# Optimization experiments

Measured on AMD Instinct MI355X. Metric: run time of the kernel, lower is better.

Reference implementation:

```python
import jax, jax.numpy as jnp
import numpy as np

B, T, V, E, H = 16, 32, 1003, 100, 2048


def setup_inputs() -> dict:
    key = jax.random.key(0)
    ks = jax.random.split(key, 16)
    s = 0.02
    n = lambda k, shape: (jax.random.normal(k, shape, jnp.float32) * s)
    tokens = jax.random.randint(ks[0], (B, T), 0, V, dtype=jnp.int32)
    return {
        "tokens": tokens,
        "emb": n(ks[1], (V, E)),
        "W1": n(ks[2], (E, 4 * H)), "U1": n(ks[3], (H, 4 * H)), "b1": jnp.zeros((4 * H,), jnp.float32),
        "W2": n(ks[4], (H, 4 * H)), "U2": n(ks[5], (H, 4 * H)), "b2": jnp.zeros((4 * H,), jnp.float32),
        "W3": n(ks[6], (H, 4 * H)), "U3": n(ks[7], (H, 4 * H)), "b3": jnp.zeros((4 * H,), jnp.float32),
        "Wd1": n(ks[8], (H, H)), "bd1": jnp.zeros((H,), jnp.float32),
        "Wd2": n(ks[9], (H, V)), "bd2": jnp.zeros((V,), jnp.float32),
    }


def masked_lstm(x, mask, W, U, b):
    """Keras-semantics masked LSTM. x: [B,T,D], mask: [B,T] bool.
    Masked steps carry h,c through unchanged (cuDNN-incompatible path).
    Returns (all_h: [B,T,H], last_h: [B,H])."""
    Hd = U.shape[0]
    Bd = x.shape[0]
    # precompute input projections for all timesteps at once: [T,B,4H]
    xz = jnp.einsum('btd,dh->tbh', x, W) + b
    m_t = jnp.swapaxes(mask, 0, 1)  # [T,B]

    def step(carry, inp):
        h, c = carry
        zx, mt = inp
        z = zx + h @ U  # [B,4H]
        i, f, g, o = jnp.split(z, 4, axis=-1)
        i = jax.nn.sigmoid(i)
        f = jax.nn.sigmoid(f)
        g = jnp.tanh(g)
        o = jax.nn.sigmoid(o)
        c_new = f * c + i * g
        h_new = o * jnp.tanh(c_new)
        m = mt[:, None]
        h_new = jnp.where(m, h_new, h)
        c_new = jnp.where(m, c_new, c)
        return (h_new, c_new), h_new

    init = (jnp.zeros((Bd, Hd), x.dtype), jnp.zeros((Bd, Hd), x.dtype))
    (h_last, _), hs = jax.lax.scan(step, init, (xz, m_t))
    return jnp.swapaxes(hs, 0, 1), h_last


def reference(tokens, emb, W1, U1, b1, W2, U2, b2, W3, U3, b3, Wd1, bd1, Wd2, bd2):
    mask = tokens != 0  # mask_zero=True semantics
    x = emb[tokens]  # [B,T,E]
    x, _ = masked_lstm(x, mask, W1, U1, b1)
    x, _ = masked_lstm(x, mask, W2, U2, b2)
    _, h = masked_lstm(x, mask, W3, U3, b3)  # return_sequences=False -> last (carried) state
    y = h @ Wd1 + bd1  # Dense, linear activation
    logits = y @ Wd2 + bd2
    return jax.nn.softmax(logits, axis=-1)
```

## Files before the change

kernel.cpp:

```cpp
#include <hip/hip_runtime.h>
#include <hip/hip_bf16.h>
#include <cstddef>

#define BB 16
#define TT 32
#define VV 1003
#define EE 100
#define HH 2048
#define G4 8192

typedef __attribute__((ext_vector_type(4))) float f32x4;
typedef unsigned char u8;

#define SA 64.0f
#define SB 128.0f
#define DESCALE 1.220703125e-4f

__device__ __forceinline__ unsigned pk_lo(unsigned old, float a, float b) {
  return (unsigned)__builtin_amdgcn_cvt_pk_fp8_f32(a, b, (int)old, false);
}
__device__ __forceinline__ unsigned pk_hi(unsigned old, float a, float b) {
  return (unsigned)__builtin_amdgcn_cvt_pk_fp8_f32(a, b, (int)old, true);
}
__device__ __forceinline__ u8 cvt1fp8(float a) {
  return (u8)(__builtin_amdgcn_cvt_pk_fp8_f32(a, 0.f, 0, false) & 0xff);
}

__global__ __launch_bounds__(256) void embed_frag(
    const int* __restrict__ tokens, const float* __restrict__ emb,
    u8* __restrict__ xf) {
  int i = blockIdx.x * 256 + threadIdx.x;
  if (i >= TT * BB * 128) return;
  int e = i & 127, b = (i >> 7) & 15, t = i >> 11;
  float v = 0.f;
  if (e < EE) v = emb[(size_t)tokens[b * TT + t] * EE + e] * SA;
  int kt = e >> 5, kk = e & 31;
  int lane = (kk >> 3) * 16 + b, j = kk & 7;
  xf[(size_t)t * 2048 + ((size_t)kt * 64 + lane) * 8 + j] = cvt1fp8(v);
}

__global__ __launch_bounds__(256) void split_fp8(
    const float* __restrict__ src, u8* __restrict__ dst,
    int Kreal, int nkt) {
  __shared__ float ld[32][257];
  int tid = threadIdx.x;
  int kt = blockIdx.x, ct0 = blockIdx.y * 16;
  int r0 = kt * 32;

#pragma unroll
  for (int i = 0; i < 8; i++) {
    int elem = i * 1024 + tid * 4;
    int row = elem >> 8, c = elem & 255;
    int g = c >> 6, rel = c & 63;
    int r = r0 + row;
    float4 v = make_float4(0.f, 0.f, 0.f, 0.f);
    if (r < Kreal)
      v = *(const float4*)&src[(size_t)r * G4 + (size_t)g * HH + ct0 * 4 + rel];
    ld[row][c] = v.x; ld[row][c + 1] = v.y;
    ld[row][c + 2] = v.z; ld[row][c + 3] = v.w;
  }
  __syncthreads();

  int L = tid & 63;
  int cl = L & 15, g = cl >> 2, hq = cl & 3;
  int row0 = (L >> 4) * 8;
#pragma unroll
  for (int pass = 0; pass < 4; pass++) {
    int ctr = (tid >> 6) + pass * 4;
    int col = g * 64 + ctr * 4 + hq;
    unsigned lo = 0, hi = 0;
    lo = pk_lo(lo, ld[row0 + 0][col] * SB, ld[row0 + 1][col] * SB);
    lo = pk_hi(lo, ld[row0 + 2][col] * SB, ld[row0 + 3][col] * SB);
    hi = pk_lo(hi, ld[row0 + 4][col] * SB, ld[row0 + 5][col] * SB);
    hi = pk_hi(hi, ld[row0 + 6][col] * SB, ld[row0 + 7][col] * SB);
    *(uint2*)&dst[((size_t)(ct0 + ctr) * nkt + kt) * 512 + L * 8] =
        make_uint2(lo, hi);
  }
}

__global__ __launch_bounds__(512) void gemm_mfma(
    const u8* __restrict__ af, int t_stride, int nkt,
    const u8* __restrict__ wfrag, const float* __restrict__ bias,
    float* __restrict__ xz) {
  __shared__ __align__(16) u8 Bs[3][2][8][512];
  int tid = threadIdx.x;
  int w = tid >> 6, L = tid & 63;
  int ct0 = blockIdx.x * 8;
  int t_a = blockIdx.y * 4 + (w & 3);
  int nt0 = (w >> 2) * 4;

  f32x4 acc[4];
#pragma unroll
  for (int i = 0; i < 4; i++) acc[i] = (f32x4){0.f, 0.f, 0.f, 0.f};
  const u8* Ah = af + (size_t)t_a * t_stride + L * 8;
  int ns = nkt >> 1;

  int tl = tid >> 5, off = (tid & 31) * 16;
  int s_nt = tl >> 1, s_kk = tl & 1;

  {
    uint4 t0 = *(const uint4*)&wfrag[((size_t)(ct0 + s_nt) * nkt + s_kk) * 512 + off];
    *(uint4*)&Bs[0][s_kk][s_nt][off] = t0;
    if (ns > 1) {
      uint4 t1 = *(const uint4*)&wfrag[((size_t)(ct0 + s_nt) * nkt + 2 + s_kk) * 512 + off];
      *(uint4*)&Bs[1][s_kk][s_nt][off] = t1;
    }
  }
  __syncthreads();

  for (int s = 0; s < ns; s++) {
    uint4 nx;
    bool pf = (s + 2 < ns);
    if (pf)
      nx = *(const uint4*)&wfrag[((size_t)(ct0 + s_nt) * nkt + 2 * (s + 2) + s_kk) * 512 + off];
    int buf = s % 3;
#pragma unroll
    for (int kk = 0; kk < 2; kk++) {
      long aH = *(const long*)(Ah + (size_t)(2 * s + kk) * 512);
#pragma unroll
      for (int i = 0; i < 4; i++) {
        long bH = *(const long*)&Bs[buf][kk][nt0 + i][L * 8];
        acc[i] = __builtin_amdgcn_mfma_f32_16x16x32_fp8_fp8(aH, bH, acc[i], 0, 0, 0);
      }
    }
    if (pf) *(uint4*)&Bs[(s + 2) % 3][s_kk][s_nt][off] = nx;
    __syncthreads();
  }

  int nq = L >> 4, hl = L & 15;
#pragma unroll
  for (int i = 0; i < 4; i++) {
    int ctg = ct0 + nt0 + i;
    int gcol = (hl >> 2) * HH + ctg * 4 + (hl & 3);
    float bv = bias[gcol];
#pragma unroll
    for (int r = 0; r < 4; r++) {
      int b = nq * 4 + r;
      xz[((size_t)t_a * 16 + b) * G4 + ctg * 16 + hl] = acc[i][r] * DESCALE + bv;
    }
  }
}

__global__ __launch_bounds__(512, 4) void lstm_step(
    const u8* __restrict__ Ufrag,
    const float* __restrict__ xzt,
    const u8* __restrict__ hf_in,
    u8* __restrict__ hf_out,
    const float* __restrict__ hT_in,
    float* __restrict__ hT_out,
    float* __restrict__ c,
    const int* __restrict__ tokens, int t) {
  __shared__ float red[8][16][16];
  __shared__ float zs[16][16];
  int tid = threadIdx.x, w = tid >> 6, L = tid & 63;
  int ct = blockIdx.x;

  float xzv = 0.f;
  if (tid < 256) xzv = xzt[(size_t)(tid >> 4) * G4 + ct * 16 + (tid & 15)];
  float c_old = 0.f, h_old = 0.f;
  int tok = 1;
  if (tid < 64) {
    int b = tid >> 2, hq = tid & 3;
    int hu = ct * 4 + hq;
    c_old = c[(size_t)b * HH + hu];
    h_old = hT_in[(size_t)hu * BB + b];
    tok = tokens[b * TT + t];
  }

  f32x4 acc = {0.f, 0.f, 0.f, 0.f};
  const u8* Ub = Ufrag + ((size_t)ct * 64 + w * 8) * 512 + L * 8;
  const u8* Hb = hf_in + (size_t)(w * 8) * 512 + L * 8;

#pragma unroll
  for (int i = 0; i < 8; i++) {
    long bh = *(const long*)(Ub + i * 512);
    long ah = *(const long*)(Hb + i * 512);
    acc = __builtin_amdgcn_mfma_f32_16x16x32_fp8_fp8(ah, bh, acc, 0, 0, 0);
  }
#pragma unroll
  for (int r = 0; r < 4; r++) red[w][(L >> 4) * 4 + r][L & 15] = acc[r];
  __syncthreads();

  if (tid < 256) {
    int b = tid >> 4, cl = tid & 15;
    float s = 0.f;
#pragma unroll
    for (int q = 0; q < 8; q++) s += red[q][b][cl];
    zs[b][cl] = s * DESCALE + xzv;
  }
  __syncthreads();

  if (tid < 64) {
    int b = tid >> 2, hq = tid & 3;
    int hu = ct * 4 + hq;
    float z0 = zs[b][0 + hq];
    float z1 = zs[b][4 + hq];
    float z2 = zs[b][8 + hq];
    float z3 = zs[b][12 + hq];
    float ig = 1.f / (1.f + expf(-z0));
    float fg = 1.f / (1.f + expf(-z1));
    float gt = tanhf(z2);
    float og = 1.f / (1.f + expf(-z3));
    float cn = fg * c_old + ig * gt;
    float hn = og * tanhf(cn);
    if (tok == 0) {
      cn = c_old;
      hn = h_old;
    }
    c[(size_t)b * HH + hu] = cn;
    hT_out[(size_t)hu * BB + b] = hn;
    int kt2 = hu >> 5, kk = hu & 31;
    int lane2 = (kk >> 3) * 16 + b, jj = kk & 7;
    hf_out[((size_t)kt2 * 64 + lane2) * 8 + jj] = cvt1fp8(hn * SA);
  }
}

__global__ __launch_bounds__(256) void head_partial(
    const float* __restrict__ XT, const float* __restrict__ W,
    float* __restrict__ partial, int N) {
  __shared__ float xs[4096];
  int tid = threadIdx.x;
  int k0 = blockIdx.y * 256;
  const float* src = XT + (size_t)k0 * 16;
  for (int i = tid; i < 4096; i += 256) xs[i] = src[i];
  __syncthreads();
  int kg = tid >> 6, lane = tid & 63;
  int col = blockIdx.x * 64 + lane;
  if (col >= N) return;
  float acc[16];
#pragma unroll
  for (int b = 0; b < 16; b++) acc[b] = 0.f;
  const float* Wp = W + (size_t)(k0 + kg * 64) * N + col;
  const float* xp = xs + kg * 64 * 16;
  for (int kk = 0; kk < 64; kk++) {
    float wv = Wp[(size_t)kk * N];
#pragma unroll
    for (int b = 0; b < 16; b++) acc[b] = fmaf(xp[kk * 16 + b], wv, acc[b]);
  }
  int chunk = blockIdx.y * 4 + kg;
#pragma unroll
  for (int b = 0; b < 16; b++)
    partial[((size_t)chunk * 16 + b) * N + col] = acc[b];
}

__global__ __launch_bounds__(256) void head_reduce(
    const float* __restrict__ partial, const float* __restrict__ bias,
    float* __restrict__ out, int N, int sc, int sb) {
  int i = blockIdx.x * 256 + threadIdx.x;
  if (i >= 16 * N) return;
  int b = i / N, col = i - b * N;
  float s = bias[col];
#pragma unroll 8
  for (int ch = 0; ch < 32; ch++) s += partial[((size_t)ch * 16 + b) * N + col];
  out[(size_t)col * sc + (size_t)b * sb] = s;
}

__global__ __launch_bounds__(256) void softmax_rows(
    const float* __restrict__ logits, float* __restrict__ out, int N) {
  __shared__ float buf[1024];
  __shared__ float wred[4];
  __shared__ float rmax, rsum;
  int b = blockIdx.x, tid = threadIdx.x;
  float m = -1e30f;
  for (int v = tid; v < N; v += 256) {
    float x = logits[(size_t)b * N + v];
    buf[v] = x;
    m = fmaxf(m, x);
  }
  for (int o = 32; o > 0; o >>= 1) m = fmaxf(m, __shfl_down(m, o, 64));
  if ((tid & 63) == 0) wred[tid >> 6] = m;
  __syncthreads();
  if (tid == 0) rmax = fmaxf(fmaxf(wred[0], wred[1]), fmaxf(wred[2], wred[3]));
  __syncthreads();
  float s = 0.f;
  for (int v = tid; v < N; v += 256) {
    float e = expf(buf[v] - rmax);
    buf[v] = e;
    s += e;
  }
  for (int o = 32; o > 0; o >>= 1) s += __shfl_down(s, o, 64);
  if ((tid & 63) == 0) wred[tid >> 6] = s;
  __syncthreads();
  if (tid == 0) rsum = wred[0] + wred[1] + wred[2] + wred[3];
  __syncthreads();
  float inv = 1.f / rsum;
  for (int v = tid; v < N; v += 256) out[(size_t)b * N + v] = buf[v] * inv;
}

extern "C" void kernel_launch(void* const* d_in, const int* in_sizes, int n_in,
                              void* d_out, int out_size, void* d_ws, size_t ws_size,
                              hipStream_t stream) {
  const int*   tokens = (const int*)d_in[0];
  const float* emb  = (const float*)d_in[1];
  const float* W1   = (const float*)d_in[2];
  const float* U1   = (const float*)d_in[3];
  const float* b1   = (const float*)d_in[4];
  const float* W2   = (const float*)d_in[5];
  const float* U2   = (const float*)d_in[6];
  const float* b2   = (const float*)d_in[7];
  const float* W3   = (const float*)d_in[8];
  const float* U3   = (const float*)d_in[9];
  const float* b3   = (const float*)d_in[10];
  const float* Wd1  = (const float*)d_in[11];
  const float* bd1  = (const float*)d_in[12];
  const float* Wd2  = (const float*)d_in[13];
  const float* bd2  = (const float*)d_in[14];
  float* out = (float*)d_out;

  char* base = (char*)d_ws;
  size_t off = 0;
  auto carve = [&](size_t bytes) -> char* {
    char* p = base + off;
    off += (bytes + 255) & ~(size_t)255;
    return p;
  };
  float* xz      = (float*)carve((size_t)TT * BB * G4 * 4);
  u8*    allhf0  = (u8*)carve(33ull * 32768);
  u8*    allhf1  = (u8*)carve(33ull * 32768);
  u8*    allhf2  = (u8*)carve(33ull * 32768);
  u8*    xfrag   = (u8*)carve((size_t)TT * 2048);
  u8*    wfrag   = (u8*)carve(512ull * 64 * 512);
  u8*    ufrag   = (u8*)carve(512ull * 64 * 512);
  float* hT0     = (float*)carve(2 * HH * BB * 4);
  float* cbuf    = hT0 + HH * BB;
  float* hT1     = (float*)carve(HH * BB * 4);
  float* yT      = (float*)carve(HH * BB * 4);
  float* logits  = (float*)carve(BB * 1024 * 4);
  float* partial = (float*)carve(32ull * 16 * HH * 4);

  u8* allhf[3] = {allhf0, allhf1, allhf2};
  const float* Us[3] = {U1, U2, U3};
  const float* Ws[3] = {W1, W2, W3};
  const float* bs[3] = {b1, b2, b3};
  float* hping[2] = {hT0, hT1};

  embed_frag<<<dim3(256), 256, 0, stream>>>(tokens, emb, xfrag);

  for (int layer = 0; layer < 3; layer++) {
    const u8* af;
    int t_stride, nktW, KrealW;
    if (layer == 0) {
      af = xfrag; t_stride = 2048; nktW = 4; KrealW = EE;
    } else {
      af = allhf[layer - 1] + 32768;
      t_stride = 32768; nktW = 64; KrealW = HH;
    }
    split_fp8<<<dim3(nktW, 32), 256, 0, stream>>>(Ws[layer], wfrag, KrealW, nktW);
    gemm_mfma<<<dim3(64, 8), 512, 0, stream>>>(
        af, t_stride, nktW, wfrag, bs[layer], xz);
    split_fp8<<<dim3(64, 32), 256, 0, stream>>>(Us[layer], ufrag, HH, 64);

    (void)hipMemsetAsync(allhf[layer], 0, 32768, stream);
    (void)hipMemsetAsync(hT0, 0, 2 * HH * BB * 4, stream);
    for (int t = 0; t < TT; t++) {
      lstm_step<<<dim3(512), 512, 0, stream>>>(
          ufrag, xz + (size_t)t * BB * G4,
          allhf[layer] + (size_t)t * 32768, allhf[layer] + (size_t)(t + 1) * 32768,
          hping[t & 1], hping[(t + 1) & 1], cbuf, tokens, t);
    }
  }

  head_partial<<<dim3(HH / 64, 8), 256, 0, stream>>>(hT0, Wd1, partial, HH);
  head_reduce<<<dim3((16 * HH + 255) / 256), 256, 0, stream>>>(partial, bd1, yT, HH, 16, 1);
  head_partial<<<dim3((VV + 63) / 64, 8), 256, 0, stream>>>(yT, Wd2, partial, VV);
  head_reduce<<<dim3((16 * VV + 255) / 256), 256, 0, stream>>>(partial, bd2, logits, VV, 1, VV);
  softmax_rows<<<dim3(BB), 256, 0, stream>>>(logits, out, VV);
}
```

Baseline: 667.0 us.

## Pair fp8 K-tiles into 16-byte fragments and split head GEMM K finer

Changes the fp8 fragment layout so each lane holds two consecutive 32-wide K tiles in 16 contiguous bytes. The split, gemm and LSTM step kernels then issue one 128-bit load per two MFMAs instead of two 64-bit loads, which cuts the load instruction count in the latency-bound recurrent step. Separately, the dense head splits K into 64 chunks instead of 32 to launch more blocks. That doubles the partial-sum buffer and the reduction work in exchange.

```diff
diff --git a/kernel.cpp b/kernel.cpp
--- a/kernel.cpp
+++ b/kernel.cpp
@@ -24,6 +24,9 @@
 }
 __device__ __forceinline__ u8 cvt1fp8(float a) {
   return (u8)(__builtin_amdgcn_cvt_pk_fp8_f32(a, 0.f, 0, false) & 0xff);
+}
+__device__ __forceinline__ long mklong(unsigned lo, unsigned hi) {
+  return (long)(((unsigned long long)hi << 32) | lo);
 }
 
 __global__ __launch_bounds__(256) void embed_frag(
@@ -36,19 +39,20 @@
   if (e < EE) v = emb[(size_t)tokens[b * TT + t] * EE + e] * SA;
   int kt = e >> 5, kk = e & 31;
   int lane = (kk >> 3) * 16 + b, j = kk & 7;
-  xf[(size_t)t * 2048 + ((size_t)kt * 64 + lane) * 8 + j] = cvt1fp8(v);
+  xf[(size_t)t * 2048 + (size_t)(kt >> 1) * 1024 + lane * 16 + (kt & 1) * 8 + j] =
+      cvt1fp8(v);
 }
 
 __global__ __launch_bounds__(256) void split_fp8(
     const float* __restrict__ src, u8* __restrict__ dst,
-    int Kreal, int nkt) {
-  __shared__ float ld[32][257];
+    int Kreal, int nkt2) {
+  __shared__ float ld[64][257];
   int tid = threadIdx.x;
-  int kt = blockIdx.x, ct0 = blockIdx.y * 16;
-  int r0 = kt * 32;
-
-#pragma unroll
-  for (int i = 0; i < 8; i++) {
+  int pair = blockIdx.x, ct0 = blockIdx.y * 16;
+  int r0 = pair * 64;
+
+#pragma unroll
+  for (int i = 0; i < 16; i++) {
     int elem = i * 1024 + tid * 4;
     int row = elem >> 8, c = elem & 255;
     int g = c >> 6, rel = c & 63;
@@ -68,21 +72,25 @@
   for (int pass = 0; pass < 4; pass++) {
     int ctr = (tid >> 6) + pass * 4;
     int col = g * 64 + ctr * 4 + hq;
-    unsigned lo = 0, hi = 0;
-    lo = pk_lo(lo, ld[row0 + 0][col] * SB, ld[row0 + 1][col] * SB);
-    lo = pk_hi(lo, ld[row0 + 2][col] * SB, ld[row0 + 3][col] * SB);
-    hi = pk_lo(hi, ld[row0 + 4][col] * SB, ld[row0 + 5][col] * SB);
-    hi = pk_hi(hi, ld[row0 + 6][col] * SB, ld[row0 + 7][col] * SB);
-    *(uint2*)&dst[((size_t)(ct0 + ctr) * nkt + kt) * 512 + L * 8] =
-        make_uint2(lo, hi);
+    unsigned lo0 = 0, hi0 = 0, lo1 = 0, hi1 = 0;
+    lo0 = pk_lo(lo0, ld[row0 + 0][col] * SB, ld[row0 + 1][col] * SB);
+    lo0 = pk_hi(lo0, ld[row0 + 2][col] * SB, ld[row0 + 3][col] * SB);
+    hi0 = pk_lo(hi0, ld[row0 + 4][col] * SB, ld[row0 + 5][col] * SB);
+    hi0 = pk_hi(hi0, ld[row0 + 6][col] * SB, ld[row0 + 7][col] * SB);
+    lo1 = pk_lo(lo1, ld[32 + row0 + 0][col] * SB, ld[32 + row0 + 1][col] * SB);
+    lo1 = pk_hi(lo1, ld[32 + row0 + 2][col] * SB, ld[32 + row0 + 3][col] * SB);
+    hi1 = pk_lo(hi1, ld[32 + row0 + 4][col] * SB, ld[32 + row0 + 5][col] * SB);
+    hi1 = pk_hi(hi1, ld[32 + row0 + 6][col] * SB, ld[32 + row0 + 7][col] * SB);
+    *(uint4*)&dst[((size_t)(ct0 + ctr) * nkt2 + pair) * 1024 + L * 16] =
+        make_uint4(lo0, hi0, lo1, hi1);
   }
 }
 
 __global__ __launch_bounds__(512) void gemm_mfma(
-    const u8* __restrict__ af, int t_stride, int nkt,
+    const u8* __restrict__ af, int t_stride, int nkt2,
     const u8* __restrict__ wfrag, const float* __restrict__ bias,
     float* __restrict__ xz) {
-  __shared__ __align__(16) u8 Bs[3][2][8][512];
+  __shared__ __align__(16) u8 Bs[3][8][1024];
   int tid = threadIdx.x;
   int w = tid >> 6, L = tid & 63;
   int ct0 = blockIdx.x * 8;
@@ -92,38 +100,35 @@
   f32x4 acc[4];
 #pragma unroll
   for (int i = 0; i < 4; i++) acc[i] = (f32x4){0.f, 0.f, 0.f, 0.f};
-  const u8* Ah = af + (size_t)t_a * t_stride + L * 8;
-  int ns = nkt >> 1;
-
-  int tl = tid >> 5, off = (tid & 31) * 16;
-  int s_nt = tl >> 1, s_kk = tl & 1;
+  const u8* Ah = af + (size_t)t_a * t_stride + L * 16;
+
+  int s_nt = tid >> 6, boff = (tid & 63) * 16;
 
   {
-    uint4 t0 = *(const uint4*)&wfrag[((size_t)(ct0 + s_nt) * nkt + s_kk) * 512 + off];
-    *(uint4*)&Bs[0][s_kk][s_nt][off] = t0;
-    if (ns > 1) {
-      uint4 t1 = *(const uint4*)&wfrag[((size_t)(ct0 + s_nt) * nkt + 2 + s_kk) * 512 + off];
-      *(uint4*)&Bs[1][s_kk][s_nt][off] = t1;
-    }
-  }
-  __syncthreads();
-
-  for (int s = 0; s < ns; s++) {
+    uint4 t0 = *(const uint4*)&wfrag[((size_t)(ct0 + s_nt) * nkt2 + 0) * 1024 + boff];
+    *(uint4*)&Bs[0][s_nt][boff] = t0;
+    if (nkt2 > 1) {
+      uint4 t1 = *(const uint4*)&wfrag[((size_t)(ct0 + s_nt) * nkt2 + 1) * 1024 + boff];
+      *(uint4*)&Bs[1][s_nt][boff] = t1;
+    }
+  }
+  __syncthreads();
+
+  for (int s = 0; s < nkt2; s++) {
     uint4 nx;
-    bool pf = (s + 2 < ns);
+    bool pf = (s + 2 < nkt2);
     if (pf)
-      nx = *(const uint4*)&wfrag[((size_t)(ct0 + s_nt) * nkt + 2 * (s + 2) + s_kk) * 512 + off];
+      nx = *(const uint4*)&wfrag[((size_t)(ct0 + s_nt) * nkt2 + s + 2) * 1024 + boff];
     int buf = s % 3;
-#pragma unroll
-    for (int kk = 0; kk < 2; kk++) {
-      long aH = *(const long*)(Ah + (size_t)(2 * s + kk) * 512);
-#pragma unroll
-      for (int i = 0; i < 4; i++) {
-        long bH = *(const long*)&Bs[buf][kk][nt0 + i][L * 8];
-        acc[i] = __builtin_amdgcn_mfma_f32_16x16x32_fp8_fp8(aH, bH, acc[i], 0, 0, 0);
-      }
-    }
-    if (pf) *(uint4*)&Bs[(s + 2) % 3][s_kk][s_nt][off] = nx;
+    uint4 a = *(const uint4*)(Ah + (size_t)s * 1024);
+    long a0 = mklong(a.x, a.y), a1 = mklong(a.z, a.w);
+#pragma unroll
+    for (int i = 0; i < 4; i++) {
+      uint4 bb = *(const uint4*)&Bs[buf][nt0 + i][L * 16];
+      acc[i] = __builtin_amdgcn_mfma_f32_16x16x32_fp8_fp8(a0, mklong(bb.x, bb.y), acc[i], 0, 0, 0);
+      acc[i] = __builtin_amdgcn_mfma_f32_16x16x32_fp8_fp8(a1, mklong(bb.z, bb.w), acc[i], 0, 0, 0);
+    }
+    if (pf) *(uint4*)&Bs[(s + 2) % 3][s_nt][boff] = nx;
     __syncthreads();
   }
 
@@ -168,14 +173,15 @@
   }
 
   f32x4 acc = {0.f, 0.f, 0.f, 0.f};
-  const u8* Ub = Ufrag + ((size_t)ct * 64 + w * 8) * 512 + L * 8;
-  const u8* Hb = hf_in + (size_t)(w * 8) * 512 + L * 8;
-
-#pragma unroll
-  for (int i = 0; i < 8; i++) {
-    long bh = *(const long*)(Ub + i * 512);
-    long ah = *(const long*)(Hb + i * 512);
-    acc = __builtin_amdgcn_mfma_f32_16x16x32_fp8_fp8(ah, bh, acc, 0, 0, 0);
+  const u8* Ub = Ufrag + ((size_t)ct * 32 + w * 4) * 1024 + L * 16;
+  const u8* Hb = hf_in + (size_t)(w * 4) * 1024 + L * 16;
+
+#pragma unroll
+  for (int i = 0; i < 4; i++) {
+    uint4 u = *(const uint4*)(Ub + i * 1024);
+    uint4 h = *(const uint4*)(Hb + i * 1024);
+    acc = __builtin_amdgcn_mfma_f32_16x16x32_fp8_fp8(mklong(h.x, h.y), mklong(u.x, u.y), acc, 0, 0, 0);
+    acc = __builtin_amdgcn_mfma_f32_16x16x32_fp8_fp8(mklong(h.z, h.w), mklong(u.z, u.w), acc, 0, 0, 0);
   }
 #pragma unroll
   for (int r = 0; r < 4; r++) red[w][(L >> 4) * 4 + r][L & 15] = acc[r];
@@ -211,18 +217,19 @@
     hT_out[(size_t)hu * BB + b] = hn;
     int kt2 = hu >> 5, kk = hu & 31;
     int lane2 = (kk >> 3) * 16 + b, jj = kk & 7;
-    hf_out[((size_t)kt2 * 64 + lane2) * 8 + jj] = cvt1fp8(hn * SA);
+    hf_out[(size_t)(kt2 >> 1) * 1024 + lane2 * 16 + (kt2 & 1) * 8 + jj] =
+        cvt1fp8(hn * SA);
   }
 }
 
 __global__ __launch_bounds__(256) void head_partial(
     const float* __restrict__ XT, const float* __restrict__ W,
     float* __restrict__ partial, int N) {
-  __shared__ float xs[4096];
+  __shared__ float xs[2048];
   int tid = threadIdx.x;
-  int k0 = blockIdx.y * 256;
+  int k0 = blockIdx.y * 128;
   const float* src = XT + (size_t)k0 * 16;
-  for (int i = tid; i < 4096; i += 256) xs[i] = src[i];
+  for (int i = tid; i < 2048; i += 256) xs[i] = src[i];
   __syncthreads();
   int kg = tid >> 6, lane = tid & 63;
   int col = blockIdx.x * 64 + lane;
@@ -230,9 +237,9 @@
   float acc[16];
 #pragma unroll
   for (int b = 0; b < 16; b++) acc[b] = 0.f;
-  const float* Wp = W + (size_t)(k0 + kg * 64) * N + col;
-  const float* xp = xs + kg * 64 * 16;
-  for (int kk = 0; kk < 64; kk++) {
+  const float* Wp = W + (size_t)(k0 + kg * 32) * N + col;
+  const float* xp = xs + kg * 32 * 16;
+  for (int kk = 0; kk < 32; kk++) {
     float wv = Wp[(size_t)kk * N];
 #pragma unroll
     for (int b = 0; b < 16; b++) acc[b] = fmaf(xp[kk * 16 + b], wv, acc[b]);
@@ -251,7 +258,7 @@
   int b = i / N, col = i - b * N;
   float s = bias[col];
 #pragma unroll 8
-  for (int ch = 0; ch < 32; ch++) s += partial[((size_t)ch * 16 + b) * N + col];
+  for (int ch = 0; ch < 64; ch++) s += partial[((size_t)ch * 16 + b) * N + col];
   out[(size_t)col * sc + (size_t)b * sb] = s;
 }
 
@@ -326,7 +333,7 @@
   float* hT1     = (float*)carve(HH * BB * 4);
   float* yT      = (float*)carve(HH * BB * 4);
   float* logits  = (float*)carve(BB * 1024 * 4);
-  float* partial = (float*)carve(32ull * 16 * HH * 4);
+  float* partial = (float*)carve(64ull * 16 * HH * 4);
 
   u8* allhf[3] = {allhf0, allhf1, allhf2};
   const float* Us[3] = {U1, U2, U3};
@@ -338,17 +345,17 @@
 
   for (int layer = 0; layer < 3; layer++) {
     const u8* af;
-    int t_stride, nktW, KrealW;
+    int t_stride, nkt2W, KrealW;
     if (layer == 0) {
-      af = xfrag; t_stride = 2048; nktW = 4; KrealW = EE;
+      af = xfrag; t_stride = 2048; nkt2W = 2; KrealW = EE;
     } else {
       af = allhf[layer - 1] + 32768;
-      t_stride = 32768; nktW = 64; KrealW = HH;
-    }
-    split_fp8<<<dim3(nktW, 32), 256, 0, stream>>>(Ws[layer], wfrag, KrealW, nktW);
+      t_stride = 32768; nkt2W = 32; KrealW = HH;
+    }
+    split_fp8<<<dim3(nkt2W, 32), 256, 0, stream>>>(Ws[layer], wfrag, KrealW, nkt2W);
     gemm_mfma<<<dim3(64, 8), 512, 0, stream>>>(
-        af, t_stride, nktW, wfrag, bs[layer], xz);
-    split_fp8<<<dim3(64, 32), 256, 0, stream>>>(Us[layer], ufrag, HH, 64);
+        af, t_stride, nkt2W, wfrag, bs[layer], xz);
+    split_fp8<<<dim3(32, 32), 256, 0, stream>>>(Us[layer], ufrag, HH, 32);
 
     (void)hipMemsetAsync(allhf[layer], 0, 32768, stream);
     (void)hipMemsetAsync(hT0, 0, 2 * HH * BB * 4, stream);
@@ -360,9 +367,9 @@
     }
   }
 
-  head_partial<<<dim3(HH / 64, 8), 256, 0, stream>>>(hT0, Wd1, partial, HH);
+  head_partial<<<dim3(HH / 64, 16), 256, 0, stream>>>(hT0, Wd1, partial, HH);
   head_reduce<<<dim3((16 * HH + 255) / 256), 256, 0, stream>>>(partial, bd1, yT, HH, 16, 1);
-  head_partial<<<dim3((VV + 63) / 64, 8), 256, 0, stream>>>(yT, Wd2, partial, VV);
+  head_partial<<<dim3((VV + 63) / 64, 16), 256, 0, stream>>>(yT, Wd2, partial, VV);
   head_reduce<<<dim3((16 * VV + 255) / 256), 256, 0, stream>>>(partial, bd2, logits, VV, 1, VV);
   softmax_rows<<<dim3(BB), 256, 0, stream>>>(logits, out, VV);
 }
```

After: 669.3 us. About the same (+0.3%).
